# Kernel optimization log

Hardware: AMD Instinct MI355X
Metric: run time of the kernel (lower is better)

The kernel has to match this reference:

```python
import jax, jax.numpy as jnp
import numpy as np

N_NODES = 200000
N_EDGES = 200000
X_SIZE = 256
H_SIZE = 256


def setup_inputs() -> dict:
    key = jax.random.key(0)
    ks = jax.random.split(key, 8)
    s = 1.0 / np.sqrt(H_SIZE)
    return {
        "x": jax.random.normal(ks[0], (N_NODES, X_SIZE), jnp.float32),
        "h": jax.random.normal(ks[1], (N_NODES, H_SIZE), jnp.float32),
        "c": jax.random.normal(ks[2], (N_NODES, H_SIZE), jnp.float32),
        "W_iou": jax.random.normal(ks[3], (3 * H_SIZE, X_SIZE), jnp.float32) * s,
        "U_iou": jax.random.normal(ks[4], (3 * H_SIZE, H_SIZE), jnp.float32) * s,
        "b_iou": jnp.zeros((1, 3 * H_SIZE), jnp.float32),
        "U_f_w": jax.random.normal(ks[5], (H_SIZE, H_SIZE), jnp.float32) * s,
        "U_f_b": jnp.zeros((H_SIZE,), jnp.float32),
        "edge_src": jax.random.randint(ks[6], (N_EDGES,), 0, N_NODES, jnp.int32),
        "edge_dst": jax.random.randint(ks[7], (N_EDGES,), 0, N_NODES, jnp.int32),
    }


def reference(x, h, c, W_iou, U_iou, b_iou, U_f_w, U_f_b, edge_src, edge_dst):
    n = x.shape[0]
    # --- message + reduce (DGL mailbox flattened to edge list) ---
    h_child = h[edge_src]                                   # [E, H] gather
    c_child = c[edge_src]                                   # [E, H]
    f = jax.nn.sigmoid(h_child @ U_f_w.T + U_f_b)           # per-child forget gate
    h_tild = jax.ops.segment_sum(h_child, edge_dst, num_segments=n)      # sum_j h_j
    c_agg = jax.ops.segment_sum(f * c_child, edge_dst, num_segments=n)   # sum_j f_j*c_j
    # --- node iou: W_iou(x) (node data) + U_iou(h_tild) from reduce ---
    iou = x @ W_iou.T + h_tild @ U_iou.T + b_iou            # [N, 3H]
    # --- apply_node_func ---
    i, o, u = jnp.split(iou, 3, axis=1)
    i = jax.nn.sigmoid(i)
    o = jax.nn.sigmoid(o)
    u = jnp.tanh(u)
    c_new = i * u + c_agg
    h_new = o * jnp.tanh(c_new)
    return h_new, c_new
```

## Files before the change

kernel.cpp:

```cpp
#include <hip/hip_runtime.h>

#define NN 200000
#define NE 200000
#define HD 256

typedef __attribute__((ext_vector_type(8))) short short8;
typedef __attribute__((ext_vector_type(4))) short short4v;
typedef __attribute__((ext_vector_type(4))) float f32x4;

static __device__ __forceinline__ unsigned short f2bf(float f) {
  unsigned u = __float_as_uint(f);
  u = (u + 0x7FFFu + ((u >> 16) & 1u)) >> 16;
  return (unsigned short)u;
}
static __device__ __forceinline__ float bf2f(unsigned short u) {
  return __uint_as_float(((unsigned)u) << 16);
}
static __device__ __forceinline__ float sigmoidf_(float x) {
  return 1.0f / (1.0f + __expf(-x));
}
static __device__ __forceinline__ float tanhf_(float x) {
  return 2.0f / (1.0f + __expf(-2.0f * x)) - 1.0f;
}
static __device__ __forceinline__ void atomAddF(float* p, float v) {
  __hip_atomic_fetch_add(p, v, __ATOMIC_RELAXED, __HIP_MEMORY_SCOPE_AGENT);
}
static __device__ __forceinline__ int atomAddI(int* p, int v) {
  return __hip_atomic_fetch_add(p, v, __ATOMIC_RELAXED, __HIP_MEMORY_SCOPE_AGENT);
}

#if __has_builtin(__builtin_amdgcn_global_load_lds)
#define HAVE_GLDS 1
static __device__ __forceinline__ void gload_lds16(const void* g, void* l) {
  __builtin_amdgcn_global_load_lds(
      (const __attribute__((address_space(1))) void*)g,
      (__attribute__((address_space(3))) void*)l, 16, 0, 0);
}
#endif

#define OFF_WFB    0u
#define OFF_BP     131072u
#define OFF_BPERM  917504u
#define OFF_ROWPTR 920576u
#define OFF_NEXT   1720832u
#define OFF_SLOT   2520832u
#define OFF_PSRC   3320832u
#define OFF_BSUM   4120832u
#define OFF_ZERO   4121856u
#define OFF_FC     4122880u
#define WS_NEED    106522880ull
#define WS_NEED_FB 1048576ull

__global__ __launch_bounds__(256) void prep_kernel(
    const float* __restrict__ Ufw, const float* __restrict__ Wiou,
    const float* __restrict__ Uiou, const float* __restrict__ biou,
    unsigned short* __restrict__ Wfb, unsigned short* __restrict__ Bp,
    float* __restrict__ bperm) {
  int idx = blockIdx.x * 256 + threadIdx.x;
  if (idx < 65536) {
    Wfb[idx] = f2bf(Ufw[idx]);
  } else if (idx < 458752) {
    int o = idx - 65536;
    int kc = o / 24576;
    int rem = o - kc * 24576;
    int tt = rem / 512;
    int rem2 = rem - tt * 512;
    int ln = rem2 >> 3, e = rem2 & 7;
    int cc = ln & 15, kgp = ln >> 4;
    int kk = kc * 32 + kgp * 8 + e;
    int g = tt % 3, tj = tt / 3;
    int orow = g * 256 + tj * 16 + cc;
    float v = (kk < 256) ? Wiou[orow * 256 + kk] : Uiou[orow * 256 + (kk - 256)];
    Bp[o] = f2bf(v);
  } else if (idx < 459520) {
    int j2 = idx - 458752;
    int T = j2 >> 4, cc = j2 & 15;
    int g = T % 3, tj = T / 3;
    bperm[j2] = biou[g * 256 + tj * 16 + cc];
  }
}

__global__ __launch_bounds__(256) void prep_fb_kernel(
    const float* __restrict__ Ufw, const float* __restrict__ Wiou,
    const float* __restrict__ Uiou, const float* __restrict__ biou,
    unsigned short* __restrict__ Wfb, unsigned short* __restrict__ Wioub,
    unsigned short* __restrict__ Uioub, float* __restrict__ bperm) {
  int idx = blockIdx.x * 256 + threadIdx.x;
  if (idx < 65536) {
    Wfb[idx] = f2bf(Ufw[idx]);
  } else if (idx < 262144) {
    int i2 = idx - 65536;
    int rp = i2 >> 8, k = i2 & 255;
    int T = rp >> 4, cc = rp & 15;
    int g = T % 3, tj = T / 3;
    Wioub[i2] = f2bf(Wiou[(g * 256 + tj * 16 + cc) * 256 + k]);
  } else if (idx < 458752) {
    int i2 = idx - 262144;
    int rp = i2 >> 8, k = i2 & 255;
    int T = rp >> 4, cc = rp & 15;
    int g = T % 3, tj = T / 3;
    Uioub[i2] = f2bf(Uiou[(g * 256 + tj * 16 + cc) * 256 + k]);
  } else if (idx < 459520) {
    int j2 = idx - 458752;
    int T = j2 >> 4, cc = j2 & 15;
    int g = T % 3, tj = T / 3;
    bperm[j2] = biou[g * 256 + tj * 16 + cc];
  }
}

__global__ __launch_bounds__(256) void hist_kernel(const int* __restrict__ edst,
                                                   int* __restrict__ cnt) {
  int e = blockIdx.x * 256 + threadIdx.x;
  if (e < NE) atomAddI(&cnt[edst[e]], 1);
}

__global__ __launch_bounds__(256) void scan_part(const int* __restrict__ cnt,
                                                 int* __restrict__ rp,
                                                 int* __restrict__ bsum) {
  __shared__ int sd[256];
  int t = threadIdx.x;
  int base = blockIdx.x * 1024 + t * 4;
  int v0 = (base + 0 < NN) ? cnt[base + 0] : 0;
  int v1 = (base + 1 < NN) ? cnt[base + 1] : 0;
  int v2 = (base + 2 < NN) ? cnt[base + 2] : 0;
  int v3 = (base + 3 < NN) ? cnt[base + 3] : 0;
  int s = v0 + v1 + v2 + v3;
  sd[t] = s;
  __syncthreads();
  for (int off = 1; off < 256; off <<= 1) {
    int add = (t >= off) ? sd[t - off] : 0;
    __syncthreads();
    sd[t] += add;
    __syncthreads();
  }
  int run = sd[t] - s;
  if (base + 0 < NN) rp[base + 0] = run; run += v0;
  if (base + 1 < NN) rp[base + 1] = run; run += v1;
  if (base + 2 < NN) rp[base + 2] = run; run += v2;
  if (base + 3 < NN) rp[base + 3] = run;
  if (t == 255) bsum[blockIdx.x] = sd[255];
}

__global__ __launch_bounds__(256) void scan_top(int* __restrict__ bsum,
                                                int* __restrict__ rp, int nb) {
  __shared__ int sd[256];
  int t = threadIdx.x;
  int v = (t < nb) ? bsum[t] : 0;
  sd[t] = v;
  __syncthreads();
  for (int off = 1; off < 256; off <<= 1) {
    int add = (t >= off) ? sd[t - off] : 0;
    __syncthreads();
    sd[t] += add;
    __syncthreads();
  }
  bsum[t] = sd[t] - v;
  if (t == 0) rp[NN] = NE;
}

__global__ __launch_bounds__(256) void scan_add(int* __restrict__ rp,
                                                const int* __restrict__ bsum,
                                                int* __restrict__ nxt) {
  int t = threadIdx.x;
  int base = blockIdx.x * 1024 + t * 4;
  int off = bsum[blockIdx.x];
#pragma unroll
  for (int j = 0; j < 4; ++j) {
    int i = base + j;
    if (i < NN) {
      int val = rp[i] + off;
      rp[i] = val;
      nxt[i] = val;
    }
  }
}

__global__ __launch_bounds__(256) void scatter_kernel(
    const int* __restrict__ esrc, const int* __restrict__ edst,
    int* __restrict__ nxt, int* __restrict__ slotArr, int* __restrict__ psrc) {
  int e = blockIdx.x * 256 + threadIdx.x;
  if (e < NE) {
    int d = edst[e];
    int pos = atomAddI(&nxt[d], 1);
    slotArr[e] = pos;
    psrc[pos] = esrc[e];
  }
}

#define F_AS 72
#define F_BS 72

__global__ __launch_bounds__(256) void edge_fc_kernel(
    const float* __restrict__ h, const float* __restrict__ c,
    const unsigned short* __restrict__ Wfb, const float* __restrict__ Ufb,
    const int* __restrict__ esrc, const int* __restrict__ slotArr,
    unsigned short* __restrict__ fcb) {
  __shared__ __align__(16) unsigned short Als[64 * F_AS];
  __shared__ __align__(16) unsigned short Bls[256 * F_BS];
  __shared__ int srcl[64], slotl[64];

  const int tid = threadIdx.x;
  const int e0 = blockIdx.x * 64;
  if (tid < 64) { srcl[tid] = esrc[e0 + tid]; slotl[tid] = slotArr[e0 + tid]; }
  __syncthreads();

  const int lane = tid & 63;
  const int wv = tid >> 6;
  const int wm = wv >> 1, wn = wv & 1;
  const int cbase = lane & 15;
  const int kg = lane >> 4;

  f32x4 acc[2][8];
#pragma unroll
  for (int i = 0; i < 2; ++i)
#pragma unroll
    for (int j = 0; j < 8; ++j) acc[i][j] = {0.f, 0.f, 0.f, 0.f};

  const int arow = tid >> 2;
  const int acg = tid & 3;
  const float* hrow = h + (size_t)srcl[arow] * HD;

  for (int kc = 0; kc < 4; ++kc) {
    const int k0 = kc * 64;
    const float4* s4 = (const float4*)(hrow + k0 + acg * 16);
    float4 q0 = s4[0], q1 = s4[1], q2 = s4[2], q3 = s4[3];
    short8 p0, p1;
    p0[0] = f2bf(q0.x); p0[1] = f2bf(q0.y); p0[2] = f2bf(q0.z); p0[3] = f2bf(q0.w);
    p0[4] = f2bf(q1.x); p0[5] = f2bf(q1.y); p0[6] = f2bf(q1.z); p0[7] = f2bf(q1.w);
    p1[0] = f2bf(q2.x); p1[1] = f2bf(q2.y); p1[2] = f2bf(q2.z); p1[3] = f2bf(q2.w);
    p1[4] = f2bf(q3.x); p1[5] = f2bf(q3.y); p1[6] = f2bf(q3.z); p1[7] = f2bf(q3.w);
    short8* ap = (short8*)&Als[arow * F_AS + acg * 16];
    ap[0] = p0; ap[1] = p1;
#pragma unroll
    for (int i = 0; i < 8; ++i) {
      int f = tid + 256 * i;
      int row = f >> 3, ch = f & 7;
      short8 vb = *(const short8*)(Wfb + row * 256 + k0 + ch * 8);
      *(short8*)&Bls[row * F_BS + ch * 8] = vb;
    }
    __syncthreads();
#pragma unroll
    for (int ks = 0; ks < 2; ++ks) {
      short8 a0 = *(const short8*)&Als[(wm * 32 + cbase) * F_AS + ks * 32 + kg * 8];
      short8 a1 = *(const short8*)&Als[(wm * 32 + 16 + cbase) * F_AS + ks * 32 + kg * 8];
#pragma unroll
      for (int nt = 0; nt < 8; ++nt) {
        short8 b = *(const short8*)&Bls[(wn * 128 + nt * 16 + cbase) * F_BS + ks * 32 + kg * 8];
        acc[0][nt] = __builtin_amdgcn_mfma_f32_16x16x32_bf16(a0, b, acc[0][nt], 0, 0, 0);
        acc[1][nt] = __builtin_amdgcn_mfma_f32_16x16x32_bf16(a1, b, acc[1][nt], 0, 0, 0);
      }
    }
    __syncthreads();
  }
  const int rsub = kg * 4;
#pragma unroll
  for (int nt = 0; nt < 8; ++nt) {
    const int coln = wn * 128 + nt * 16 + cbase;
    const float bias = Ufb[coln];
#pragma unroll
    for (int mt = 0; mt < 2; ++mt) {
#pragma unroll
      for (int j = 0; j < 4; ++j) {
        const int el = wm * 32 + mt * 16 + rsub + j;
        const float fg = sigmoidf_(acc[mt][nt][j] + bias);
        const float cv = c[(size_t)srcl[el] * HD + coln];
        fcb[(size_t)slotl[el] * HD + coln] = f2bf(fg * cv);
      }
    }
  }
}

__global__ __launch_bounds__(256) void gather_kernel(
    const float* __restrict__ h, const int* __restrict__ rp,
    const int* __restrict__ psrc, unsigned short* __restrict__ fcb,
    float* __restrict__ cagg) {
  const int tid = threadIdx.x;
  const int node = blockIdx.x * 32 + (tid >> 3);
  const int cg = tid & 7;
  const int s0 = rp[node], s1 = rp[node + 1];

  float hs[32], cs[32];
#pragma unroll
  for (int q = 0; q < 32; ++q) { hs[q] = 0.f; cs[q] = 0.f; }

  for (int s = s0; s < s1; ++s) {
    const int src = psrc[s];
    const float4* hp = (const float4*)(h + (size_t)src * HD + cg * 32);
    const short8* fp = (const short8*)(fcb + (size_t)s * HD + cg * 32);
#pragma unroll
    for (int q = 0; q < 8; ++q) {
      float4 v = hp[q];
      hs[4 * q + 0] += v.x; hs[4 * q + 1] += v.y;
      hs[4 * q + 2] += v.z; hs[4 * q + 3] += v.w;
    }
#pragma unroll
    for (int q = 0; q < 4; ++q) {
      short8 w = fp[q];
#pragma unroll
      for (int e = 0; e < 8; ++e) cs[8 * q + e] += bf2f((unsigned short)w[e]);
    }
  }
  float4* cp = (float4*)(cagg + (size_t)node * HD + cg * 32);
#pragma unroll
  for (int q = 0; q < 8; ++q) {
    float4 v = {cs[4 * q + 0], cs[4 * q + 1], cs[4 * q + 2], cs[4 * q + 3]};
    cp[q] = v;
  }
  if (s1 > s0) {
    short8* hd = (short8*)(fcb + (size_t)s0 * HD + cg * 32);
#pragma unroll
    for (int q = 0; q < 4; ++q) {
      short8 p;
#pragma unroll
      for (int e = 0; e < 8; ++e) p[e] = f2bf(hs[8 * q + e]);
      hd[q] = p;
    }
  }
}

__global__ __launch_bounds__(512, 4) void iou_gemm_kernel(
    const float* __restrict__ x, const unsigned short* __restrict__ Bp,
    const float* __restrict__ bperm, const int* __restrict__ rp,
    const unsigned short* __restrict__ fcb, const char* __restrict__ zpage,
    float* __restrict__ out) {
  __shared__ __align__(16) unsigned short Bls[48 * 512];

  const int tid = threadIdx.x;
  const int lane = tid & 63;
  const int wv = tid >> 6;
  const int wm = wv >> 2, wn = wv & 3;
  const int cbase = lane & 15;
  const int kg = lane >> 4;
  const int r0 = blockIdx.x * 64;
  const int row0 = r0 + wm * 32 + cbase;
  const int row1 = row0 + 16;

  const int sa0 = rp[row0], ea0 = rp[row0 + 1];
  const int sa1 = rp[row1], ea1 = rp[row1 + 1];
  const char* pH0 = (ea0 > sa0) ? (const char*)(fcb + (size_t)sa0 * HD) : zpage;
  const char* pH1 = (ea1 > sa1) ? (const char*)(fcb + (size_t)sa1 * HD) : zpage;
  const float* pX0 = x + (size_t)row0 * HD;
  const float* pX1 = x + (size_t)row1 * HD;

  f32x4 acc[2][12];
#pragma unroll
  for (int m = 0; m < 2; ++m)
#pragma unroll
    for (int t = 0; t < 12; ++t) acc[m][t] = {0.f, 0.f, 0.f, 0.f};

  for (int kc = 0; kc < 16; ++kc) {
    const char* gB = (const char*)Bp + kc * 49152 + wv * 1024 + lane * 16;
    char* lB = (char*)Bls + wv * 1024;
#ifdef HAVE_GLDS
#pragma unroll
    for (int i = 0; i < 6; ++i) gload_lds16(gB + i * 8192, lB + i * 8192);
#else
#pragma unroll
    for (int i = 0; i < 6; ++i) {
      short8 v = *(const short8*)(gB + i * 8192);
      *(short8*)(lB + lane * 16 + i * 8192) = v;
    }
#endif
    short8 a0, a1;
    const int k0 = (kc & 7) * 32;
    if (kc < 8) {
      float4 u0 = *(const float4*)(pX0 + k0 + kg * 8);
      float4 u1 = *(const float4*)(pX0 + k0 + kg * 8 + 4);
      float4 u2 = *(const float4*)(pX1 + k0 + kg * 8);
      float4 u3 = *(const float4*)(pX1 + k0 + kg * 8 + 4);
      a0[0] = f2bf(u0.x); a0[1] = f2bf(u0.y); a0[2] = f2bf(u0.z); a0[3] = f2bf(u0.w);
      a0[4] = f2bf(u1.x); a0[5] = f2bf(u1.y); a0[6] = f2bf(u1.z); a0[7] = f2bf(u1.w);
      a1[0] = f2bf(u2.x); a1[1] = f2bf(u2.y); a1[2] = f2bf(u2.z); a1[3] = f2bf(u2.w);
      a1[4] = f2bf(u3.x); a1[5] = f2bf(u3.y); a1[6] = f2bf(u3.z); a1[7] = f2bf(u3.w);
    } else {
      a0 = *(const short8*)(pH0 + k0 * 2 + kg * 16);
      a1 = *(const short8*)(pH1 + k0 * 2 + kg * 16);
    }
    __syncthreads();
    const char* bbase = (const char*)Bls + (wn * 12) * 1024 + lane * 16;
#pragma unroll
    for (int tt = 0; tt < 12; ++tt) {
      short8 b = *(const short8*)(bbase + tt * 1024);
      acc[0][tt] = __builtin_amdgcn_mfma_f32_16x16x32_bf16(a0, b, acc[0][tt], 0, 0, 0);
      acc[1][tt] = __builtin_amdgcn_mfma_f32_16x16x32_bf16(a1, b, acc[1][tt], 0, 0, 0);
    }
    __syncthreads();
  }

  float* outc = out + (size_t)NN * HD;
  const int rbase = wm * 32 + kg * 4;
#pragma unroll
  for (int t3 = 0; t3 < 4; ++t3) {
    const int T = wn * 12 + 3 * t3;
    const float bi = bperm[(T + 0) * 16 + cbase];
    const float bo = bperm[(T + 1) * 16 + cbase];
    const float bu = bperm[(T + 2) * 16 + cbase];
    const int j = (wn * 4 + t3) * 16 + cbase;
#pragma unroll
    for (int mf = 0; mf < 2; ++mf) {
#pragma unroll
      for (int jr = 0; jr < 4; ++jr) {
        const int rl = rbase + mf * 16 + jr;
        const size_t idx = (size_t)(r0 + rl) * HD + j;
        const float iv = sigmoidf_(acc[mf][3 * t3 + 0][jr] + bi);
        const float ov = sigmoidf_(acc[mf][3 * t3 + 1][jr] + bo);
        const float uv = tanhf_(acc[mf][3 * t3 + 2][jr] + bu);
        const float cn = iv * uv + outc[idx];
        out[idx] = ov * tanhf_(cn);
        outc[idx] = cn;
      }
    }
  }
}

__global__ __launch_bounds__(256) void edge_kernel(
    const float* __restrict__ h, const float* __restrict__ c,
    const unsigned short* __restrict__ Wfb, const float* __restrict__ Ufb,
    const int* __restrict__ esrc, const int* __restrict__ edst,
    float* h_tild, float* c_agg) {
  __shared__ __align__(16) unsigned short Als[64 * F_AS];
  __shared__ __align__(16) unsigned short Bls[256 * F_BS];
  __shared__ int srcl[64], dstl[64];

  const int tid = threadIdx.x;
  const int e0 = blockIdx.x * 64;
  if (tid < 64) { srcl[tid] = esrc[e0 + tid]; dstl[tid] = edst[e0 + tid]; }
  __syncthreads();

  const int lane = tid & 63;
  const int wv = tid >> 6;
  const int wm = wv >> 1, wn = wv & 1;
  const int cbase = lane & 15;
  const int kg = lane >> 4;

  f32x4 acc[2][8];
#pragma unroll
  for (int i = 0; i < 2; ++i)
#pragma unroll
    for (int j = 0; j < 8; ++j) acc[i][j] = {0.f, 0.f, 0.f, 0.f};

  const int arow = tid >> 2;
  const int acg = tid & 3;
  const float* hrow = h + (size_t)srcl[arow] * HD;
  float* htrow = h_tild + (size_t)dstl[arow] * HD;

  for (int kc = 0; kc < 4; ++kc) {
    const int k0 = kc * 64;
    const float4* s4 = (const float4*)(hrow + k0 + acg * 16);
    float4 q0 = s4[0], q1 = s4[1], q2 = s4[2], q3 = s4[3];
    short8 p0, p1;
    p0[0] = f2bf(q0.x); p0[1] = f2bf(q0.y); p0[2] = f2bf(q0.z); p0[3] = f2bf(q0.w);
    p0[4] = f2bf(q1.x); p0[5] = f2bf(q1.y); p0[6] = f2bf(q1.z); p0[7] = f2bf(q1.w);
    p1[0] = f2bf(q2.x); p1[1] = f2bf(q2.y); p1[2] = f2bf(q2.z); p1[3] = f2bf(q2.w);
    p1[4] = f2bf(q3.x); p1[5] = f2bf(q3.y); p1[6] = f2bf(q3.z); p1[7] = f2bf(q3.w);
    short8* ap = (short8*)&Als[arow * F_AS + acg * 16];
    ap[0] = p0; ap[1] = p1;
    {
      float* hp = htrow + k0 + acg * 16;
      atomAddF(hp + 0, q0.x);  atomAddF(hp + 1, q0.y);
      atomAddF(hp + 2, q0.z);  atomAddF(hp + 3, q0.w);
      atomAddF(hp + 4, q1.x);  atomAddF(hp + 5, q1.y);
      atomAddF(hp + 6, q1.z);  atomAddF(hp + 7, q1.w);
      atomAddF(hp + 8, q2.x);  atomAddF(hp + 9, q2.y);
      atomAddF(hp + 10, q2.z); atomAddF(hp + 11, q2.w);
      atomAddF(hp + 12, q3.x); atomAddF(hp + 13, q3.y);
      atomAddF(hp + 14, q3.z); atomAddF(hp + 15, q3.w);
    }
#pragma unroll
    for (int i = 0; i < 8; ++i) {
      int f = tid + 256 * i;
      int row = f >> 3, ch = f & 7;
      short8 vb = *(const short8*)(Wfb + row * 256 + k0 + ch * 8);
      *(short8*)&Bls[row * F_BS + ch * 8] = vb;
    }
    __syncthreads();
#pragma unroll
    for (int ks = 0; ks < 2; ++ks) {
      short8 a0 = *(const short8*)&Als[(wm * 32 + cbase) * F_AS + ks * 32 + kg * 8];
      short8 a1 = *(const short8*)&Als[(wm * 32 + 16 + cbase) * F_AS + ks * 32 + kg * 8];
#pragma unroll
      for (int nt = 0; nt < 8; ++nt) {
        short8 b = *(const short8*)&Bls[(wn * 128 + nt * 16 + cbase) * F_BS + ks * 32 + kg * 8];
        acc[0][nt] = __builtin_amdgcn_mfma_f32_16x16x32_bf16(a0, b, acc[0][nt], 0, 0, 0);
        acc[1][nt] = __builtin_amdgcn_mfma_f32_16x16x32_bf16(a1, b, acc[1][nt], 0, 0, 0);
      }
    }
    __syncthreads();
  }
  const int rsub = kg * 4;
#pragma unroll
  for (int nt = 0; nt < 8; ++nt) {
    const int coln = wn * 128 + nt * 16 + cbase;
    const float bias = Ufb[coln];
#pragma unroll
    for (int mt = 0; mt < 2; ++mt) {
#pragma unroll
      for (int j = 0; j < 4; ++j) {
        const int el = wm * 32 + mt * 16 + rsub + j;
        const float fg = sigmoidf_(acc[mt][nt][j] + bias);
        const float cv = c[(size_t)srcl[el] * HD + coln];
        atomAddF(c_agg + (size_t)dstl[el] * HD + coln, fg * cv);
      }
    }
  }
}

#define I_AS 40
#define I_BS 40

__global__ __launch_bounds__(256) void iou_kernel(
    const float* __restrict__ x, const unsigned short* __restrict__ Wioub,
    const unsigned short* __restrict__ Uioub, const float* __restrict__ bperm,
    float* out) {
  __shared__ __align__(16) unsigned short Als[32 * I_AS];
  __shared__ __align__(16) unsigned short Bls[768 * I_BS];

  const int tid = threadIdx.x;
  const int lane = tid & 63;
  const int wv = tid >> 6;
  const int wm = wv >> 1, wn = wv & 1;
  const int cbase = lane & 15;
  const int kg = lane >> 4;
  const int r0 = blockIdx.x * 32;

  float* h_tild = out;
  float* c_agg = out + (size_t)NN * HD;

  f32x4 acc[24];
#pragma unroll
  for (int t = 0; t < 24; ++t) acc[t] = {0.f, 0.f, 0.f, 0.f};

  const int arow = tid >> 3;
  const int acg = tid & 7;

  for (int pass = 0; pass < 2; ++pass) {
    const float* As = pass ? h_tild : x;
    const unsigned short* Bs = pass ? Uioub : Wioub;
    for (int kc = 0; kc < 8; ++kc) {
      const int k0 = kc * 32;
      float4 q = *(const float4*)(As + (size_t)(r0 + arow) * HD + k0 + acg * 4);
      short4v p;
      p[0] = f2bf(q.x); p[1] = f2bf(q.y); p[2] = f2bf(q.z); p[3] = f2bf(q.w);
      *(short4v*)&Als[arow * I_AS + acg * 4] = p;
#pragma unroll
      for (int i = 0; i < 12; ++i) {
        int f = tid + 256 * i;
        int row = f >> 2, ch = f & 3;
        short8 vb = *(const short8*)(Bs + row * 256 + k0 + ch * 8);
        *(short8*)&Bls[row * I_BS + ch * 8] = vb;
      }
      __syncthreads();
      short8 a = *(const short8*)&Als[(wm * 16 + cbase) * I_AS + kg * 8];
#pragma unroll
      for (int tt = 0; tt < 24; ++tt) {
        short8 b = *(const short8*)&Bls[((wn * 24 + tt) * 16 + cbase) * I_BS + kg * 8];
        acc[tt] = __builtin_amdgcn_mfma_f32_16x16x32_bf16(a, b, acc[tt], 0, 0, 0);
      }
      __syncthreads();
    }
  }
  const int rsub = kg * 4;
#pragma unroll
  for (int t3 = 0; t3 < 8; ++t3) {
    const int T = wn * 24 + 3 * t3;
    const float bi = bperm[(T + 0) * 16 + cbase];
    const float bo = bperm[(T + 1) * 16 + cbase];
    const float bu = bperm[(T + 2) * 16 + cbase];
    const int j = (wn * 8 + t3) * 16 + cbase;
#pragma unroll
    for (int jr = 0; jr < 4; ++jr) {
      const int r = r0 + wm * 16 + rsub + jr;
      const size_t idx = (size_t)r * HD + j;
      const float iv = sigmoidf_(acc[3 * t3 + 0][jr] + bi);
      const float ov = sigmoidf_(acc[3 * t3 + 1][jr] + bo);
      const float uv = tanhf_(acc[3 * t3 + 2][jr] + bu);
      const float cn = iv * uv + c_agg[idx];
      out[idx] = ov * tanhf_(cn);
      c_agg[idx] = cn;
    }
  }
}

extern "C" void kernel_launch(void* const* d_in, const int* in_sizes, int n_in,
                              void* d_out, int out_size, void* d_ws, size_t ws_size,
                              hipStream_t stream) {
  const float* x    = (const float*)d_in[0];
  const float* h    = (const float*)d_in[1];
  const float* c    = (const float*)d_in[2];
  const float* Wiou = (const float*)d_in[3];
  const float* Uiou = (const float*)d_in[4];
  const float* biou = (const float*)d_in[5];
  const float* Ufw  = (const float*)d_in[6];
  const float* Ufb  = (const float*)d_in[7];
  const int* esrc   = (const int*)d_in[8];
  const int* edst   = (const int*)d_in[9];
  float* out = (float*)d_out;

  char* ws = (char*)d_ws;
  unsigned short* Wfb   = (unsigned short*)(ws + OFF_WFB);
  unsigned short* Bp    = (unsigned short*)(ws + OFF_BP);
  float* bperm          = (float*)(ws + OFF_BPERM);

  if (ws_size >= WS_NEED) {
    int* rpp  = (int*)(ws + OFF_ROWPTR);
    int* nxt  = (int*)(ws + OFF_NEXT);
    int* slot = (int*)(ws + OFF_SLOT);
    int* psrc = (int*)(ws + OFF_PSRC);
    int* bsum = (int*)(ws + OFF_BSUM);
    char* zpage = ws + OFF_ZERO;
    unsigned short* fcb = (unsigned short*)(ws + OFF_FC);

    hipMemsetAsync(nxt, 0, (size_t)NN * sizeof(int), stream);
    hipMemsetAsync(zpage, 0, 1024, stream);
    prep_kernel<<<1795, 256, 0, stream>>>(Ufw, Wiou, Uiou, biou, Wfb, Bp, bperm);
    hist_kernel<<<(NE + 255) / 256, 256, 0, stream>>>(edst, nxt);
    scan_part<<<(NN + 1023) / 1024, 256, 0, stream>>>(nxt, rpp, bsum);
    scan_top<<<1, 256, 0, stream>>>(bsum, rpp, (NN + 1023) / 1024);
    scan_add<<<(NN + 1023) / 1024, 256, 0, stream>>>(rpp, bsum, nxt);
    scatter_kernel<<<(NE + 255) / 256, 256, 0, stream>>>(esrc, edst, nxt, slot, psrc);
    edge_fc_kernel<<<NE / 64, 256, 0, stream>>>(h, c, Wfb, Ufb, esrc, slot, fcb);
    gather_kernel<<<NN / 32, 256, 0, stream>>>(h, rpp, psrc, fcb, out + (size_t)NN * HD);
    iou_gemm_kernel<<<NN / 64, 512, 0, stream>>>(x, Bp, bperm, rpp, fcb, zpage, out);
  } else {
    unsigned short* Wioub = (unsigned short*)(ws + OFF_BP);
    unsigned short* Uioub = (unsigned short*)(ws + OFF_BP + 393216);
    hipMemsetAsync(d_out, 0, (size_t)out_size * sizeof(float), stream);
    prep_fb_kernel<<<1795, 256, 0, stream>>>(Ufw, Wiou, Uiou, biou, Wfb, Wioub, Uioub, bperm);
    edge_kernel<<<NE / 64, 256, 0, stream>>>(h, c, Wfb, Ufb, esrc, edst,
                                             out, out + (size_t)NN * HD);
    iou_kernel<<<NN / 32, 256, 0, stream>>>(x, Wioub, Uioub, bperm, out);
  }
}
```

Measured before the change: 849.5 us.

## Double-buffer B tiles and prefetch A fragments in the iou GEMM

The iou GEMM now keeps two LDS buffers for the B tile. It issues the global-to-LDS load for chunk kc+1, together with the register prefetch of the next x or h fragment, before running the MFMAs on chunk kc. This drops one barrier per iteration and hides global load latency behind compute. LDS use doubles to 96 KB per block, and the launch bound occupancy hint drops from 4 to 2 blocks per CU, so fewer waves are resident to hide latency. The non-GLDS fallback path is removed.

```diff
diff --git a/kernel.cpp b/kernel.cpp
--- a/kernel.cpp
+++ b/kernel.cpp
@@ -29,13 +29,14 @@
   return __hip_atomic_fetch_add(p, v, __ATOMIC_RELAXED, __HIP_MEMORY_SCOPE_AGENT);
 }
 
-#if __has_builtin(__builtin_amdgcn_global_load_lds)
-#define HAVE_GLDS 1
+#if defined(__HIP_DEVICE_COMPILE__)
 static __device__ __forceinline__ void gload_lds16(const void* g, void* l) {
   __builtin_amdgcn_global_load_lds(
       (const __attribute__((address_space(1))) void*)g,
       (__attribute__((address_space(3))) void*)l, 16, 0, 0);
 }
+#else
+static __device__ __forceinline__ void gload_lds16(const void*, void*) {}
 #endif
 
 #define OFF_WFB    0u
@@ -49,7 +50,6 @@
 #define OFF_ZERO   4121856u
 #define OFF_FC     4122880u
 #define WS_NEED    106522880ull
-#define WS_NEED_FB 1048576ull
 
 __global__ __launch_bounds__(256) void prep_kernel(
     const float* __restrict__ Ufw, const float* __restrict__ Wiou,
@@ -318,12 +318,12 @@
   }
 }
 
-__global__ __launch_bounds__(512, 4) void iou_gemm_kernel(
+__global__ __launch_bounds__(512, 2) void iou_gemm_kernel(
     const float* __restrict__ x, const unsigned short* __restrict__ Bp,
     const float* __restrict__ bperm, const int* __restrict__ rp,
     const unsigned short* __restrict__ fcb, const char* __restrict__ zpage,
     float* __restrict__ out) {
-  __shared__ __align__(16) unsigned short Bls[48 * 512];
+  __shared__ __align__(16) unsigned short Bls[2][48 * 512];
 
   const int tid = threadIdx.x;
   const int lane = tid & 63;
@@ -348,36 +348,55 @@
 #pragma unroll
     for (int t = 0; t < 12; ++t) acc[m][t] = {0.f, 0.f, 0.f, 0.f};
 
+  float4 xr0, xr1, xr2, xr3;
+  short8 hr0, hr1;
+
+#define STAGE_B(KC, BUF)                                                      \
+  do {                                                                        \
+    const char* gB_ = (const char*)Bp + (KC)*49152 + wv * 1024 + lane * 16;   \
+    char* lB_ = (char*)Bls[BUF] + wv * 1024;                                  \
+    _Pragma("unroll")                                                         \
+    for (int i_ = 0; i_ < 6; ++i_) gload_lds16(gB_ + i_ * 8192, lB_ + i_ * 8192); \
+  } while (0)
+
+#define LOADA_X(KC)                                                           \
+  do {                                                                        \
+    const int k0_ = (KC)*32;                                                  \
+    xr0 = *(const float4*)(pX0 + k0_ + kg * 8);                               \
+    xr1 = *(const float4*)(pX0 + k0_ + kg * 8 + 4);                           \
+    xr2 = *(const float4*)(pX1 + k0_ + kg * 8);                               \
+    xr3 = *(const float4*)(pX1 + k0_ + kg * 8 + 4);                           \
+  } while (0)
+
+#define LOADA_H(KC)                                                           \
+  do {                                                                        \
+    const int k0_ = ((KC)-8) * 32;                                            \
+    hr0 = *(const short8*)(pH0 + k0_ * 2 + kg * 16);                          \
+    hr1 = *(const short8*)(pH1 + k0_ * 2 + kg * 16);                          \
+  } while (0)
+
+  STAGE_B(0, 0);
+  LOADA_X(0);
+  __syncthreads();
+
   for (int kc = 0; kc < 16; ++kc) {
-    const char* gB = (const char*)Bp + kc * 49152 + wv * 1024 + lane * 16;
-    char* lB = (char*)Bls + wv * 1024;
-#ifdef HAVE_GLDS
-#pragma unroll
-    for (int i = 0; i < 6; ++i) gload_lds16(gB + i * 8192, lB + i * 8192);
-#else
-#pragma unroll
-    for (int i = 0; i < 6; ++i) {
-      short8 v = *(const short8*)(gB + i * 8192);
-      *(short8*)(lB + lane * 16 + i * 8192) = v;
-    }
-#endif
+    const int cur = kc & 1;
     short8 a0, a1;
-    const int k0 = (kc & 7) * 32;
     if (kc < 8) {
-      float4 u0 = *(const float4*)(pX0 + k0 + kg * 8);
-      float4 u1 = *(const float4*)(pX0 + k0 + kg * 8 + 4);
-      float4 u2 = *(const float4*)(pX1 + k0 + kg * 8);
-      float4 u3 = *(const float4*)(pX1 + k0 + kg * 8 + 4);
-      a0[0] = f2bf(u0.x); a0[1] = f2bf(u0.y); a0[2] = f2bf(u0.z); a0[3] = f2bf(u0.w);
-      a0[4] = f2bf(u1.x); a0[5] = f2bf(u1.y); a0[6] = f2bf(u1.z); a0[7] = f2bf(u1.w);
-      a1[0] = f2bf(u2.x); a1[1] = f2bf(u2.y); a1[2] = f2bf(u2.z); a1[3] = f2bf(u2.w);
-      a1[4] = f2bf(u3.x); a1[5] = f2bf(u3.y); a1[6] = f2bf(u3.z); a1[7] = f2bf(u3.w);
+      a0[0] = f2bf(xr0.x); a0[1] = f2bf(xr0.y); a0[2] = f2bf(xr0.z); a0[3] = f2bf(xr0.w);
+      a0[4] = f2bf(xr1.x); a0[5] = f2bf(xr1.y); a0[6] = f2bf(xr1.z); a0[7] = f2bf(xr1.w);
+      a1[0] = f2bf(xr2.x); a1[1] = f2bf(xr2.y); a1[2] = f2bf(xr2.z); a1[3] = f2bf(xr2.w);
+      a1[4] = f2bf(xr3.x); a1[5] = f2bf(xr3.y); a1[6] = f2bf(xr3.z); a1[7] = f2bf(xr3.w);
     } else {
-      a0 = *(const short8*)(pH0 + k0 * 2 + kg * 16);
-      a1 = *(const short8*)(pH1 + k0 * 2 + kg * 16);
-    }
-    __syncthreads();
-    const char* bbase = (const char*)Bls + (wn * 12) * 1024 + lane * 16;
+      a0 = hr0;
+      a1 = hr1;
+    }
+    if (kc < 15) {
+      STAGE_B(kc + 1, cur ^ 1);
+      if (kc + 1 < 8) LOADA_X(kc + 1);
+      else            LOADA_H(kc + 1);
+    }
+    const char* bbase = (const char*)Bls[cur] + (wn * 12) * 1024 + lane * 16;
 #pragma unroll
     for (int tt = 0; tt < 12; ++tt) {
       short8 b = *(const short8*)(bbase + tt * 1024);
@@ -386,6 +405,10 @@
     }
     __syncthreads();
   }
+
+#undef STAGE_B
+#undef LOADA_X
+#undef LOADA_H
 
   float* outc = out + (size_t)NN * HD;
   const int rbase = wm * 32 + kg * 4;
@@ -610,8 +633,8 @@
     char* zpage = ws + OFF_ZERO;
     unsigned short* fcb = (unsigned short*)(ws + OFF_FC);
 
-    hipMemsetAsync(nxt, 0, (size_t)NN * sizeof(int), stream);
-    hipMemsetAsync(zpage, 0, 1024, stream);
+    (void)hipMemsetAsync(nxt, 0, (size_t)NN * sizeof(int), stream);
+    (void)hipMemsetAsync(zpage, 0, 1024, stream);
     prep_kernel<<<1795, 256, 0, stream>>>(Ufw, Wiou, Uiou, biou, Wfb, Bp, bperm);
     hist_kernel<<<(NE + 255) / 256, 256, 0, stream>>>(edst, nxt);
     scan_part<<<(NN + 1023) / 1024, 256, 0, stream>>>(nxt, rpp, bsum);
@@ -624,7 +647,7 @@
   } else {
     unsigned short* Wioub = (unsigned short*)(ws + OFF_BP);
     unsigned short* Uioub = (unsigned short*)(ws + OFF_BP + 393216);
-    hipMemsetAsync(d_out, 0, (size_t)out_size * sizeof(float), stream);
+    (void)hipMemsetAsync(d_out, 0, (size_t)out_size * sizeof(float), stream);
     prep_fb_kernel<<<1795, 256, 0, stream>>>(Ufw, Wiou, Uiou, biou, Wfb, Wioub, Uioub, bperm);
     edge_kernel<<<NE / 64, 256, 0, stream>>>(h, c, Wfb, Ufb, esrc, edst,
                                              out, out + (size_t)NN * HD);
```

Result: slower. 973.9 us (+14.6%).

## Split IOU GEMM N-dimension across two blocks and stream B fragments via registers

Applied to the files above, without the earlier changes.

The IOU GEMM now launches twice as many blocks, each computing half of the 768 output columns for a 64-row tile. The shared-memory B staging and its two barriers per k-step are removed; each wave loads its B fragments straight from global memory into registers, double-buffered with the next step's x/h operand loads. This targets barrier stalls and LDS traffic and raises occupancy. In exchange, every row group reads x and the h aggregate twice, and B is fetched per wave from L2 without sharing inside the block.

```diff
diff --git a/kernel.cpp b/kernel.cpp
--- a/kernel.cpp
+++ b/kernel.cpp
@@ -28,15 +28,6 @@
 static __device__ __forceinline__ int atomAddI(int* p, int v) {
   return __hip_atomic_fetch_add(p, v, __ATOMIC_RELAXED, __HIP_MEMORY_SCOPE_AGENT);
 }
-
-#if __has_builtin(__builtin_amdgcn_global_load_lds)
-#define HAVE_GLDS 1
-static __device__ __forceinline__ void gload_lds16(const void* g, void* l) {
-  __builtin_amdgcn_global_load_lds(
-      (const __attribute__((address_space(1))) void*)g,
-      (__attribute__((address_space(3))) void*)l, 16, 0, 0);
-}
-#endif
 
 #define OFF_WFB    0u
 #define OFF_BP     131072u
@@ -49,7 +40,6 @@
 #define OFF_ZERO   4121856u
 #define OFF_FC     4122880u
 #define WS_NEED    106522880ull
-#define WS_NEED_FB 1048576ull
 
 __global__ __launch_bounds__(256) void prep_kernel(
     const float* __restrict__ Ufw, const float* __restrict__ Wiou,
@@ -318,20 +308,22 @@
   }
 }
 
-__global__ __launch_bounds__(512, 4) void iou_gemm_kernel(
+__global__ __launch_bounds__(512) void iou_gemm_kernel(
     const float* __restrict__ x, const unsigned short* __restrict__ Bp,
     const float* __restrict__ bperm, const int* __restrict__ rp,
     const unsigned short* __restrict__ fcb, const char* __restrict__ zpage,
     float* __restrict__ out) {
-  __shared__ __align__(16) unsigned short Bls[48 * 512];
-
   const int tid = threadIdx.x;
   const int lane = tid & 63;
   const int wv = tid >> 6;
   const int wm = wv >> 2, wn = wv & 3;
   const int cbase = lane & 15;
   const int kg = lane >> 4;
-  const int r0 = blockIdx.x * 64;
+
+  const int bid = blockIdx.x;
+  const int rgrp = bid >> 1;
+  const int nh = bid & 1;
+  const int r0 = rgrp * 64;
   const int row0 = r0 + wm * 32 + cbase;
   const int row1 = row0 + 16;
 
@@ -342,60 +334,71 @@
   const float* pX0 = x + (size_t)row0 * HD;
   const float* pX1 = x + (size_t)row1 * HD;
 
-  f32x4 acc[2][12];
+  const char* pB = (const char*)Bp + ((size_t)(nh * 24 + wn * 6) * 64 + lane) * 16;
+
+  f32x4 acc[2][6];
 #pragma unroll
   for (int m = 0; m < 2; ++m)
 #pragma unroll
-    for (int t = 0; t < 12; ++t) acc[m][t] = {0.f, 0.f, 0.f, 0.f};
-
+    for (int t = 0; t < 6; ++t) acc[m][t] = {0.f, 0.f, 0.f, 0.f};
+
+  short8 Bf[2][6];
+  float4 Xr[2][4];
+  short8 Hr[2][2];
+
+#pragma unroll
+  for (int t = 0; t < 6; ++t) Bf[0][t] = *(const short8*)(pB + t * 1024);
+  Xr[0][0] = *(const float4*)(pX0 + kg * 8);
+  Xr[0][1] = *(const float4*)(pX0 + kg * 8 + 4);
+  Xr[0][2] = *(const float4*)(pX1 + kg * 8);
+  Xr[0][3] = *(const float4*)(pX1 + kg * 8 + 4);
+
+#pragma unroll
   for (int kc = 0; kc < 16; ++kc) {
-    const char* gB = (const char*)Bp + kc * 49152 + wv * 1024 + lane * 16;
-    char* lB = (char*)Bls + wv * 1024;
-#ifdef HAVE_GLDS
-#pragma unroll
-    for (int i = 0; i < 6; ++i) gload_lds16(gB + i * 8192, lB + i * 8192);
-#else
-#pragma unroll
-    for (int i = 0; i < 6; ++i) {
-      short8 v = *(const short8*)(gB + i * 8192);
-      *(short8*)(lB + lane * 16 + i * 8192) = v;
-    }
-#endif
+    const int cur = kc & 1, nxt = cur ^ 1;
+    if (kc < 15) {
+      const char* pBn = pB + (kc + 1) * 49152;
+#pragma unroll
+      for (int t = 0; t < 6; ++t) Bf[nxt][t] = *(const short8*)(pBn + t * 1024);
+      if (kc + 1 < 8) {
+        const int k0n = (kc + 1) * 32;
+        Xr[nxt][0] = *(const float4*)(pX0 + k0n + kg * 8);
+        Xr[nxt][1] = *(const float4*)(pX0 + k0n + kg * 8 + 4);
+        Xr[nxt][2] = *(const float4*)(pX1 + k0n + kg * 8);
+        Xr[nxt][3] = *(const float4*)(pX1 + k0n + kg * 8 + 4);
+      } else {
+        const int k0n = (kc + 1 - 8) * 32;
+        Hr[nxt][0] = *(const short8*)(pH0 + k0n * 2 + kg * 16);
+        Hr[nxt][1] = *(const short8*)(pH1 + k0n * 2 + kg * 16);
+      }
+    }
     short8 a0, a1;
-    const int k0 = (kc & 7) * 32;
     if (kc < 8) {
-      float4 u0 = *(const float4*)(pX0 + k0 + kg * 8);
-      float4 u1 = *(const float4*)(pX0 + k0 + kg * 8 + 4);
-      float4 u2 = *(const float4*)(pX1 + k0 + kg * 8);
-      float4 u3 = *(const float4*)(pX1 + k0 + kg * 8 + 4);
+      float4 u0 = Xr[cur][0], u1 = Xr[cur][1], u2 = Xr[cur][2], u3 = Xr[cur][3];
       a0[0] = f2bf(u0.x); a0[1] = f2bf(u0.y); a0[2] = f2bf(u0.z); a0[3] = f2bf(u0.w);
       a0[4] = f2bf(u1.x); a0[5] = f2bf(u1.y); a0[6] = f2bf(u1.z); a0[7] = f2bf(u1.w);
       a1[0] = f2bf(u2.x); a1[1] = f2bf(u2.y); a1[2] = f2bf(u2.z); a1[3] = f2bf(u2.w);
       a1[4] = f2bf(u3.x); a1[5] = f2bf(u3.y); a1[6] = f2bf(u3.z); a1[7] = f2bf(u3.w);
     } else {
-      a0 = *(const short8*)(pH0 + k0 * 2 + kg * 16);
-      a1 = *(const short8*)(pH1 + k0 * 2 + kg * 16);
-    }
-    __syncthreads();
-    const char* bbase = (const char*)Bls + (wn * 12) * 1024 + lane * 16;
-#pragma unroll
-    for (int tt = 0; tt < 12; ++tt) {
-      short8 b = *(const short8*)(bbase + tt * 1024);
-      acc[0][tt] = __builtin_amdgcn_mfma_f32_16x16x32_bf16(a0, b, acc[0][tt], 0, 0, 0);
-      acc[1][tt] = __builtin_amdgcn_mfma_f32_16x16x32_bf16(a1, b, acc[1][tt], 0, 0, 0);
-    }
-    __syncthreads();
+      a0 = Hr[cur][0];
+      a1 = Hr[cur][1];
+    }
+#pragma unroll
+    for (int tt = 0; tt < 6; ++tt) {
+      acc[0][tt] = __builtin_amdgcn_mfma_f32_16x16x32_bf16(a0, Bf[cur][tt], acc[0][tt], 0, 0, 0);
+      acc[1][tt] = __builtin_amdgcn_mfma_f32_16x16x32_bf16(a1, Bf[cur][tt], acc[1][tt], 0, 0, 0);
+    }
   }
 
   float* outc = out + (size_t)NN * HD;
   const int rbase = wm * 32 + kg * 4;
 #pragma unroll
-  for (int t3 = 0; t3 < 4; ++t3) {
-    const int T = wn * 12 + 3 * t3;
-    const float bi = bperm[(T + 0) * 16 + cbase];
-    const float bo = bperm[(T + 1) * 16 + cbase];
-    const float bu = bperm[(T + 2) * 16 + cbase];
-    const int j = (wn * 4 + t3) * 16 + cbase;
+  for (int t3 = 0; t3 < 2; ++t3) {
+    const int TT = nh * 24 + wn * 6 + 3 * t3;
+    const float bi = bperm[(TT + 0) * 16 + cbase];
+    const float bo = bperm[(TT + 1) * 16 + cbase];
+    const float bu = bperm[(TT + 2) * 16 + cbase];
+    const int j = (nh * 8 + wn * 2 + t3) * 16 + cbase;
 #pragma unroll
     for (int mf = 0; mf < 2; ++mf) {
 #pragma unroll
@@ -610,8 +613,8 @@
     char* zpage = ws + OFF_ZERO;
     unsigned short* fcb = (unsigned short*)(ws + OFF_FC);
 
-    hipMemsetAsync(nxt, 0, (size_t)NN * sizeof(int), stream);
-    hipMemsetAsync(zpage, 0, 1024, stream);
+    (void)hipMemsetAsync(nxt, 0, (size_t)NN * sizeof(int), stream);
+    (void)hipMemsetAsync(zpage, 0, 1024, stream);
     prep_kernel<<<1795, 256, 0, stream>>>(Ufw, Wiou, Uiou, biou, Wfb, Bp, bperm);
     hist_kernel<<<(NE + 255) / 256, 256, 0, stream>>>(edst, nxt);
     scan_part<<<(NN + 1023) / 1024, 256, 0, stream>>>(nxt, rpp, bsum);
@@ -620,11 +623,11 @@
     scatter_kernel<<<(NE + 255) / 256, 256, 0, stream>>>(esrc, edst, nxt, slot, psrc);
     edge_fc_kernel<<<NE / 64, 256, 0, stream>>>(h, c, Wfb, Ufb, esrc, slot, fcb);
     gather_kernel<<<NN / 32, 256, 0, stream>>>(h, rpp, psrc, fcb, out + (size_t)NN * HD);
-    iou_gemm_kernel<<<NN / 64, 512, 0, stream>>>(x, Bp, bperm, rpp, fcb, zpage, out);
+    iou_gemm_kernel<<<6250, 512, 0, stream>>>(x, Bp, bperm, rpp, fcb, zpage, out);
   } else {
     unsigned short* Wioub = (unsigned short*)(ws + OFF_BP);
     unsigned short* Uioub = (unsigned short*)(ws + OFF_BP + 393216);
-    hipMemsetAsync(d_out, 0, (size_t)out_size * sizeof(float), stream);
+    (void)hipMemsetAsync(d_out, 0, (size_t)out_size * sizeof(float), stream);
     prep_fb_kernel<<<1795, 256, 0, stream>>>(Ufw, Wiou, Uiou, biou, Wfb, Wioub, Uioub, bperm);
     edge_kernel<<<NE / 64, 256, 0, stream>>>(h, c, Wfb, Ufb, esrc, edst,
                                              out, out + (size_t)NN * HD);
```

After: 985.2 us. 1.16x slower.

## Retile IOU GEMM to 128-row blocks split over four column quarters with LDS-staged A

Applied to the files above, without the earlier changes.

The IOU GEMM kernel is restructured from 64-row, 512-thread blocks that compute all 768 output columns into 256-thread blocks that each cover 128 rows and one quarter of the columns, giving four times as many blocks. The A operand (x rows and the aggregated h rows) is now staged into LDS with direct global-to-LDS loads and an XOR swizzle, rather than being loaded straight into registers per lane. The aim is more parallelism and asynchronous, coalesced A loads that reduce bank conflicts. In exchange, each x row is re-read by four blocks (one per column quarter), and the loop still has no double buffering, so loads are not overlapped with compute.

```diff
diff --git a/kernel.cpp b/kernel.cpp
--- a/kernel.cpp
+++ b/kernel.cpp
@@ -29,13 +29,14 @@
   return __hip_atomic_fetch_add(p, v, __ATOMIC_RELAXED, __HIP_MEMORY_SCOPE_AGENT);
 }
 
-#if __has_builtin(__builtin_amdgcn_global_load_lds)
-#define HAVE_GLDS 1
+#if defined(__HIP_DEVICE_COMPILE__)
 static __device__ __forceinline__ void gload_lds16(const void* g, void* l) {
   __builtin_amdgcn_global_load_lds(
       (const __attribute__((address_space(1))) void*)g,
       (__attribute__((address_space(3))) void*)l, 16, 0, 0);
 }
+#else
+static __device__ __forceinline__ void gload_lds16(const void*, void*) {}
 #endif
 
 #define OFF_WFB    0u
@@ -49,7 +50,6 @@
 #define OFF_ZERO   4121856u
 #define OFF_FC     4122880u
 #define WS_NEED    106522880ull
-#define WS_NEED_FB 1048576ull
 
 __global__ __launch_bounds__(256) void prep_kernel(
     const float* __restrict__ Ufw, const float* __restrict__ Wiou,
@@ -318,29 +318,45 @@
   }
 }
 
-__global__ __launch_bounds__(512, 4) void iou_gemm_kernel(
+__global__ __launch_bounds__(256) void iou_gemm4_kernel(
     const float* __restrict__ x, const unsigned short* __restrict__ Bp,
     const float* __restrict__ bperm, const int* __restrict__ rp,
     const unsigned short* __restrict__ fcb, const char* __restrict__ zpage,
     float* __restrict__ out) {
-  __shared__ __align__(16) unsigned short Bls[48 * 512];
+  __shared__ __align__(16) unsigned char Als[16384];
+  __shared__ __align__(16) unsigned char Bls[12288];
 
   const int tid = threadIdx.x;
   const int lane = tid & 63;
   const int wv = tid >> 6;
-  const int wm = wv >> 2, wn = wv & 3;
   const int cbase = lane & 15;
   const int kg = lane >> 4;
-  const int r0 = blockIdx.x * 64;
-  const int row0 = r0 + wm * 32 + cbase;
-  const int row1 = row0 + 16;
-
-  const int sa0 = rp[row0], ea0 = rp[row0 + 1];
-  const int sa1 = rp[row1], ea1 = rp[row1 + 1];
-  const char* pH0 = (ea0 > sa0) ? (const char*)(fcb + (size_t)sa0 * HD) : zpage;
-  const char* pH1 = (ea1 > sa1) ? (const char*)(fcb + (size_t)sa1 * HD) : zpage;
-  const float* pX0 = x + (size_t)row0 * HD;
-  const float* pX1 = x + (size_t)row1 * HD;
+
+  const int bid = blockIdx.x;
+  const int rgrp = bid >> 2;
+  const int nq = bid & 3;
+  const int r0 = rgrp * 128;
+
+  const int cI = lane & 7;
+  const int rbase = wv * 8 + (lane >> 3);
+  const int offX = (cI * 16) ^ ((rbase & 7) << 4);
+  const char* xsrc[4];
+#pragma unroll
+  for (int i = 0; i < 4; ++i) {
+    int rr = r0 + rbase + i * 32; if (rr > NN - 1) rr = NN - 1;
+    xsrc[i] = (const char*)x + (size_t)rr * 1024 + offX;
+  }
+  const int cH = lane & 3;
+  const char* hsrc[2];
+#pragma unroll
+  for (int i = 0; i < 2; ++i) {
+    const int rl = i * 64 + wv * 16 + (lane >> 2);
+    int rr = r0 + rl; if (rr > NN - 1) rr = NN - 1;
+    const int s0 = rp[rr], s1 = rp[rr + 1];
+    const char* base = (s1 > s0) ? (const char*)(fcb + (size_t)s0 * HD) : zpage;
+    hsrc[i] = base + ((cH * 16) ^ ((rl & 3) << 4));
+  }
+  const char* bsrc = (const char*)Bp + (size_t)nq * 12288 + (wv * 64 + lane) * 16;
 
   f32x4 acc[2][12];
 #pragma unroll
@@ -348,39 +364,45 @@
 #pragma unroll
     for (int t = 0; t < 12; ++t) acc[m][t] = {0.f, 0.f, 0.f, 0.f};
 
+  const int frow0 = wv * 32 + cbase;
+  const int swX = (frow0 & 7) << 4;
+  const int swH = (frow0 & 3) << 4;
+
   for (int kc = 0; kc < 16; ++kc) {
-    const char* gB = (const char*)Bp + kc * 49152 + wv * 1024 + lane * 16;
-    char* lB = (char*)Bls + wv * 1024;
-#ifdef HAVE_GLDS
-#pragma unroll
-    for (int i = 0; i < 6; ++i) gload_lds16(gB + i * 8192, lB + i * 8192);
-#else
-#pragma unroll
-    for (int i = 0; i < 6; ++i) {
-      short8 v = *(const short8*)(gB + i * 8192);
-      *(short8*)(lB + lane * 16 + i * 8192) = v;
-    }
-#endif
+#pragma unroll
+    for (int i = 0; i < 3; ++i)
+      gload_lds16(bsrc + (size_t)kc * 49152 + i * 4096,
+                  Bls + i * 4096 + wv * 1024);
+    if (kc < 8) {
+#pragma unroll
+      for (int i = 0; i < 4; ++i)
+        gload_lds16(xsrc[i] + kc * 128, Als + i * 4096 + wv * 1024);
+    } else {
+#pragma unroll
+      for (int i = 0; i < 2; ++i)
+        gload_lds16(hsrc[i] + (kc - 8) * 64, Als + i * 4096 + wv * 1024);
+    }
+    __syncthreads();
+
     short8 a0, a1;
-    const int k0 = (kc & 7) * 32;
     if (kc < 8) {
-      float4 u0 = *(const float4*)(pX0 + k0 + kg * 8);
-      float4 u1 = *(const float4*)(pX0 + k0 + kg * 8 + 4);
-      float4 u2 = *(const float4*)(pX1 + k0 + kg * 8);
-      float4 u3 = *(const float4*)(pX1 + k0 + kg * 8 + 4);
-      a0[0] = f2bf(u0.x); a0[1] = f2bf(u0.y); a0[2] = f2bf(u0.z); a0[3] = f2bf(u0.w);
-      a0[4] = f2bf(u1.x); a0[5] = f2bf(u1.y); a0[6] = f2bf(u1.z); a0[7] = f2bf(u1.w);
-      a1[0] = f2bf(u2.x); a1[1] = f2bf(u2.y); a1[2] = f2bf(u2.z); a1[3] = f2bf(u2.w);
-      a1[4] = f2bf(u3.x); a1[5] = f2bf(u3.y); a1[6] = f2bf(u3.z); a1[7] = f2bf(u3.w);
+      const unsigned char* ar0 = Als + frow0 * 128;
+      const unsigned char* ar1 = Als + (frow0 + 16) * 128;
+      float4 q0 = *(const float4*)(ar0 + ((kg * 32) ^ swX));
+      float4 q1 = *(const float4*)(ar0 + ((kg * 32 + 16) ^ swX));
+      float4 q2 = *(const float4*)(ar1 + ((kg * 32) ^ swX));
+      float4 q3 = *(const float4*)(ar1 + ((kg * 32 + 16) ^ swX));
+      a0[0] = f2bf(q0.x); a0[1] = f2bf(q0.y); a0[2] = f2bf(q0.z); a0[3] = f2bf(q0.w);
+      a0[4] = f2bf(q1.x); a0[5] = f2bf(q1.y); a0[6] = f2bf(q1.z); a0[7] = f2bf(q1.w);
+      a1[0] = f2bf(q2.x); a1[1] = f2bf(q2.y); a1[2] = f2bf(q2.z); a1[3] = f2bf(q2.w);
+      a1[4] = f2bf(q3.x); a1[5] = f2bf(q3.y); a1[6] = f2bf(q3.z); a1[7] = f2bf(q3.w);
     } else {
-      a0 = *(const short8*)(pH0 + k0 * 2 + kg * 16);
-      a1 = *(const short8*)(pH1 + k0 * 2 + kg * 16);
-    }
-    __syncthreads();
-    const char* bbase = (const char*)Bls + (wn * 12) * 1024 + lane * 16;
+      a0 = *(const short8*)(Als + frow0 * 64 + ((kg * 16) ^ swH));
+      a1 = *(const short8*)(Als + (frow0 + 16) * 64 + ((kg * 16) ^ swH));
+    }
 #pragma unroll
     for (int tt = 0; tt < 12; ++tt) {
-      short8 b = *(const short8*)(bbase + tt * 1024);
+      short8 b = *(const short8*)(Bls + tt * 1024 + lane * 16);
       acc[0][tt] = __builtin_amdgcn_mfma_f32_16x16x32_bf16(a0, b, acc[0][tt], 0, 0, 0);
       acc[1][tt] = __builtin_amdgcn_mfma_f32_16x16x32_bf16(a1, b, acc[1][tt], 0, 0, 0);
     }
@@ -388,26 +410,28 @@
   }
 
   float* outc = out + (size_t)NN * HD;
-  const int rbase = wm * 32 + kg * 4;
 #pragma unroll
   for (int t3 = 0; t3 < 4; ++t3) {
-    const int T = wn * 12 + 3 * t3;
-    const float bi = bperm[(T + 0) * 16 + cbase];
-    const float bo = bperm[(T + 1) * 16 + cbase];
-    const float bu = bperm[(T + 2) * 16 + cbase];
-    const int j = (wn * 4 + t3) * 16 + cbase;
+    const int TT = nq * 12 + 3 * t3;
+    const float bi = bperm[(TT + 0) * 16 + cbase];
+    const float bo = bperm[(TT + 1) * 16 + cbase];
+    const float bu = bperm[(TT + 2) * 16 + cbase];
+    const int j = (nq * 4 + t3) * 16 + cbase;
 #pragma unroll
     for (int mf = 0; mf < 2; ++mf) {
 #pragma unroll
       for (int jr = 0; jr < 4; ++jr) {
-        const int rl = rbase + mf * 16 + jr;
-        const size_t idx = (size_t)(r0 + rl) * HD + j;
-        const float iv = sigmoidf_(acc[mf][3 * t3 + 0][jr] + bi);
-        const float ov = sigmoidf_(acc[mf][3 * t3 + 1][jr] + bo);
-        const float uv = tanhf_(acc[mf][3 * t3 + 2][jr] + bu);
-        const float cn = iv * uv + outc[idx];
-        out[idx] = ov * tanhf_(cn);
-        outc[idx] = cn;
+        const int rl = wv * 32 + mf * 16 + kg * 4 + jr;
+        const int gr = r0 + rl;
+        if (gr < NN) {
+          const size_t idx = (size_t)gr * HD + j;
+          const float iv = sigmoidf_(acc[mf][3 * t3 + 0][jr] + bi);
+          const float ov = sigmoidf_(acc[mf][3 * t3 + 1][jr] + bo);
+          const float uv = tanhf_(acc[mf][3 * t3 + 2][jr] + bu);
+          const float cn = iv * uv + outc[idx];
+          out[idx] = ov * tanhf_(cn);
+          outc[idx] = cn;
+        }
       }
     }
   }
@@ -610,8 +634,8 @@
     char* zpage = ws + OFF_ZERO;
     unsigned short* fcb = (unsigned short*)(ws + OFF_FC);
 
-    hipMemsetAsync(nxt, 0, (size_t)NN * sizeof(int), stream);
-    hipMemsetAsync(zpage, 0, 1024, stream);
+    (void)hipMemsetAsync(nxt, 0, (size_t)NN * sizeof(int), stream);
+    (void)hipMemsetAsync(zpage, 0, 1024, stream);
     prep_kernel<<<1795, 256, 0, stream>>>(Ufw, Wiou, Uiou, biou, Wfb, Bp, bperm);
     hist_kernel<<<(NE + 255) / 256, 256, 0, stream>>>(edst, nxt);
     scan_part<<<(NN + 1023) / 1024, 256, 0, stream>>>(nxt, rpp, bsum);
@@ -620,11 +644,12 @@
     scatter_kernel<<<(NE + 255) / 256, 256, 0, stream>>>(esrc, edst, nxt, slot, psrc);
     edge_fc_kernel<<<NE / 64, 256, 0, stream>>>(h, c, Wfb, Ufb, esrc, slot, fcb);
     gather_kernel<<<NN / 32, 256, 0, stream>>>(h, rpp, psrc, fcb, out + (size_t)NN * HD);
-    iou_gemm_kernel<<<NN / 64, 512, 0, stream>>>(x, Bp, bperm, rpp, fcb, zpage, out);
+    const int rgrps = (NN + 127) / 128;
+    iou_gemm4_kernel<<<rgrps * 4, 256, 0, stream>>>(x, Bp, bperm, rpp, fcb, zpage, out);
   } else {
     unsigned short* Wioub = (unsigned short*)(ws + OFF_BP);
     unsigned short* Uioub = (unsigned short*)(ws + OFF_BP + 393216);
-    hipMemsetAsync(d_out, 0, (size_t)out_size * sizeof(float), stream);
+    (void)hipMemsetAsync(d_out, 0, (size_t)out_size * sizeof(float), stream);
     prep_fb_kernel<<<1795, 256, 0, stream>>>(Ufw, Wiou, Uiou, biou, Wfb, Wioub, Uioub, bperm);
     edge_kernel<<<NE / 64, 256, 0, stream>>>(h, c, Wfb, Ufb, esrc, edst,
                                              out, out + (size_t)NN * HD);
```

After: 870.5 us. +2.5%, slower.
